# Performance work log

Measured on AMD Instinct MI355X. Metric: run time of the kernel, lower is better.

The kernel has to match this reference:

```python
import jax, jax.numpy as jnp
import numpy as np

B, S, H, L = 128, 2048, 512, 11

def setup_inputs() -> dict:
    key = jax.random.key(0)
    k1, k2, k3, k4 = jax.random.split(key, 4)
    return {
        "find_contri": 1,
        "code_output": jax.random.normal(k1, (B, S, H), dtype=jnp.float32),
        "lengths": jax.random.randint(k2, (B,), 1, S + 1),  # ragged lengths in [1, S]
        "contri": jax.random.uniform(k3, (B, S, 2), dtype=jnp.float32),
        "fc_w": jax.random.normal(k4, (L, H), dtype=jnp.float32) * 0.05,
    }

def reference(find_contri, code_output, lengths, contri, fc_w):
    b, s, h = code_output.shape
    # Faithful to torch .view (reshape, not transpose): [B,S,H] -> [B,H,S]
    x = code_output.reshape(b, h, s)
    # Ragged adaptive max-pool to size 1 with indices: mask positions >= length
    valid = jnp.arange(s)[None, :] < lengths[:, None]            # [B,S]
    xm = jnp.where(valid[:, None, :], x, -jnp.inf)               # [B,H,S]
    code_pool = jnp.max(xm, axis=2)                              # [B,H]
    code_indices = jnp.argmax(xm, axis=2)                        # [B,H], in [0,len)
    attn = code_pool @ fc_w.T                                    # [B,11], no bias
    if find_contri:
        # con[lab,i] = relu(pool[i]*fc_w[lab]) + 1e-4, normalized to sum 100.
        # Original mutates one `contri` tensor across all labs and appends the
        # same reference 11 times; the final state is the sum over labs.
        p10 = code_pool[:10]                                     # only first 10 samples
        con = jax.nn.relu(p10[:, None, :] * fc_w[None, :, :]) + 1e-4   # [10,11,H]
        con = con / jnp.sum(con, axis=2, keepdims=True) * 100.0
        total = jnp.sum(con, axis=1)                             # [10,H]
        # indexed scatter-add into the new third channel
        scat = jax.vmap(lambda idx, c: jnp.zeros((s,), total.dtype).at[idx].add(c))(
            code_indices[:10], total)                            # [10,S]
        ch2 = jnp.zeros((b, s), contri.dtype).at[:10].set(scat)  # [B,S]
        contri_out = jnp.concatenate([contri, ch2[..., None]], axis=2)  # [B,S,3]
        return attn, contri_out
    return attn
```

## Files before the change

kernel.cpp:

```cpp
#include <hip/hip_runtime.h>
#include <math.h>

#define BB 128
#define SS 2048
#define HH 512
#define LL 11

__global__ __launch_bounds__(256) void rowmax_kernel(
    const float* __restrict__ x,
    const int* __restrict__ lengths,
    float* __restrict__ pool,
    int* __restrict__ idx_out) {
  int gid = blockIdx.x * blockDim.x + threadIdx.x;
  int wave = gid >> 6;
  int lane = threadIdx.x & 63;
  if (wave >= BB * HH) return;
  int b = wave >> 9;
  int len = lengths[b];
  const float4* row = (const float4*)(x + (size_t)wave * SS);

  float best = -INFINITY;
  int bidx = 0;
#pragma unroll
  for (int j = 0; j < 8; ++j) {
    int e = j * 64 + lane;
    float4 v = row[e];
    int si = e * 4;
    float a;
    a = (si + 0 < len) ? v.x : -INFINITY;
    if (a > best) { best = a; bidx = si + 0; }
    a = (si + 1 < len) ? v.y : -INFINITY;
    if (a > best) { best = a; bidx = si + 1; }
    a = (si + 2 < len) ? v.z : -INFINITY;
    if (a > best) { best = a; bidx = si + 2; }
    a = (si + 3 < len) ? v.w : -INFINITY;
    if (a > best) { best = a; bidx = si + 3; }
  }
#pragma unroll
  for (int off = 32; off > 0; off >>= 1) {
    float ov = __shfl_down(best, off);
    int oi = __shfl_down(bidx, off);
    if (ov > best || (ov == best && oi < bidx)) { best = ov; bidx = oi; }
  }
  if (lane == 0) {
    pool[wave] = best;
    idx_out[wave] = bidx;
  }
}

__global__ __launch_bounds__(256) void attn_kernel(
    const float* __restrict__ pool,
    const float* __restrict__ fcw,
    float* __restrict__ attn_out) {
  int gid = blockIdx.x * blockDim.x + threadIdx.x;
  int wid = gid >> 6;
  int lane = threadIdx.x & 63;
  if (wid >= BB * LL) return;
  int b = wid / LL;
  int l = wid - b * LL;
  const float* p = pool + b * HH;
  const float* w = fcw + l * HH;
  float sum = 0.f;
#pragma unroll
  for (int k = 0; k < HH / 64; ++k) sum += p[k * 64 + lane] * w[k * 64 + lane];
#pragma unroll
  for (int off = 32; off > 0; off >>= 1) sum += __shfl_down(sum, off);
  if (lane == 0) attn_out[wid] = sum;
}

__global__ __launch_bounds__(256) void denom_kernel(
    const float* __restrict__ pool,
    const float* __restrict__ fcw,
    float* __restrict__ denom) {
  int gid = blockIdx.x * blockDim.x + threadIdx.x;
  int wid = gid >> 6;
  int lane = threadIdx.x & 63;
  if (wid >= 10 * LL) return;
  int b = wid / LL;
  int l = wid - b * LL;
  const float* p = pool + b * HH;
  const float* w = fcw + l * HH;
  float sum = 0.f;
#pragma unroll
  for (int k = 0; k < HH / 64; ++k)
    sum += fmaxf(p[k * 64 + lane] * w[k * 64 + lane], 0.f);
#pragma unroll
  for (int off = 32; off > 0; off >>= 1) sum += __shfl_down(sum, off);
  if (lane == 0) denom[wid] = sum + (float)HH * 1e-4f;
}

__global__ __launch_bounds__(512) void scatter_kernel(
    const float* __restrict__ pool,
    const float* __restrict__ fcw,
    const float* __restrict__ denom,
    const int* __restrict__ idx_in,
    float* __restrict__ ch2) {
  int b = blockIdx.x;
  int hh = threadIdx.x;
  __shared__ float sden[LL];
  if (threadIdx.x < LL) sden[threadIdx.x] = 100.f / denom[b * LL + threadIdx.x];
  __syncthreads();
  float p = pool[b * HH + hh];
  float total = 0.f;
#pragma unroll
  for (int l = 0; l < LL; ++l) {
    float c = fmaxf(p * fcw[l * HH + hh], 0.f) + 1e-4f;
    total += c * sden[l];
  }
  atomicAdd(&ch2[b * SS + idx_in[b * HH + hh]], total);
}

__global__ __launch_bounds__(256) void finalize_kernel(
    const float* __restrict__ contri,
    const float* __restrict__ ch2,
    float* __restrict__ out2) {
  int t = blockIdx.x * blockDim.x + threadIdx.x;
  if (t >= BB * SS) return;
  float c0 = contri[t * 2 + 0];
  float c1 = contri[t * 2 + 1];
  float c2 = (t < 10 * SS) ? ch2[t] : 0.f;
  out2[t * 3 + 0] = c0;
  out2[t * 3 + 1] = c1;
  out2[t * 3 + 2] = c2;
}

extern "C" void kernel_launch(void* const* d_in, const int* in_sizes, int n_in,
                              void* d_out, int out_size, void* d_ws, size_t ws_size,
                              hipStream_t stream) {
  const float* code_output = (const float*)d_in[1];
  const int* lengths = (const int*)d_in[2];
  const float* contri = (const float*)d_in[3];
  const float* fcw = (const float*)d_in[4];

  float* out = (float*)d_out;
  float* out2 = out + BB * LL;

  float* ws = (float*)d_ws;
  float* pool = ws;
  int* idx = (int*)(ws + 65536);
  float* denom = ws + 131072;
  float* ch2 = ws + 131200;

  hipMemsetAsync(ch2, 0, (size_t)10 * SS * sizeof(float), stream);

  rowmax_kernel<<<(BB * HH * 64) / 256, 256, 0, stream>>>(code_output, lengths,
                                                          pool, idx);
  attn_kernel<<<(BB * LL * 64 + 255) / 256, 256, 0, stream>>>(pool, fcw, out);
  denom_kernel<<<(10 * LL * 64 + 255) / 256, 256, 0, stream>>>(pool, fcw, denom);
  scatter_kernel<<<10, 512, 0, stream>>>(pool, fcw, denom, idx, ch2);
  finalize_kernel<<<(BB * SS + 255) / 256, 256, 0, stream>>>(contri, ch2, out2);
}
```

Before: 691.3 us.

## Fuse attn, denom, scatter and finalize into one epilogue kernel; nontemporal row loads

Merges the four small post-reduction kernels and the memset into a single epilogue launch. Block roles are split by block index: the first 10 blocks compute denominators, scatter-add into shared memory and write the contri rows for the first 10 samples; the next 128 blocks compute attn; the remaining blocks copy contri and write zeros. The rowmax streaming loads become nontemporal. This removes several launches plus the global atomic and memset round trips, in exchange for more complex per-block branching and shared-memory atomics.

```diff
diff --git a/kernel.cpp b/kernel.cpp
--- a/kernel.cpp
+++ b/kernel.cpp
@@ -5,6 +5,8 @@
 #define SS 2048
 #define HH 512
 #define LL 11
+
+typedef float vf4 __attribute__((ext_vector_type(4)));
 
 __global__ __launch_bounds__(256) void rowmax_kernel(
     const float* __restrict__ x,
@@ -17,14 +19,14 @@
   if (wave >= BB * HH) return;
   int b = wave >> 9;
   int len = lengths[b];
-  const float4* row = (const float4*)(x + (size_t)wave * SS);
+  const vf4* row = (const vf4*)(x + (size_t)wave * SS);
 
   float best = -INFINITY;
   int bidx = 0;
 #pragma unroll
   for (int j = 0; j < 8; ++j) {
     int e = j * 64 + lane;
-    float4 v = row[e];
+    vf4 v = __builtin_nontemporal_load(&row[e]);
     int si = e * 4;
     float a;
     a = (si + 0 < len) ? v.x : -INFINITY;
@@ -48,80 +50,77 @@
   }
 }
 
-__global__ __launch_bounds__(256) void attn_kernel(
+__global__ __launch_bounds__(256) void epilogue_kernel(
     const float* __restrict__ pool,
+    const int* __restrict__ idx_in,
     const float* __restrict__ fcw,
-    float* __restrict__ attn_out) {
-  int gid = blockIdx.x * blockDim.x + threadIdx.x;
-  int wid = gid >> 6;
-  int lane = threadIdx.x & 63;
-  if (wid >= BB * LL) return;
-  int b = wid / LL;
-  int l = wid - b * LL;
-  const float* p = pool + b * HH;
-  const float* w = fcw + l * HH;
-  float sum = 0.f;
+    const float* __restrict__ contri,
+    float* __restrict__ attn_out,
+    float* __restrict__ out2) {
+  int tid = threadIdx.x;
+  int wv = tid >> 6;
+  int lane = tid & 63;
+
+  if (blockIdx.x < 10) {
+    int b = blockIdx.x;
+    __shared__ float sp[HH];
+    __shared__ float sden[LL];
+    __shared__ float sch[SS];
+
+    for (int h = tid; h < HH; h += 256) sp[h] = pool[b * HH + h];
+    for (int s = tid; s < SS; s += 256) sch[s] = 0.f;
+    __syncthreads();
+
+    for (int l = wv; l < LL; l += 4) {
+      float s = 0.f;
 #pragma unroll
-  for (int k = 0; k < HH / 64; ++k) sum += p[k * 64 + lane] * w[k * 64 + lane];
+      for (int k = 0; k < HH / 64; ++k) {
+        int h = k * 64 + lane;
+        s += fmaxf(sp[h] * fcw[l * HH + h], 0.f);
+      }
 #pragma unroll
-  for (int off = 32; off > 0; off >>= 1) sum += __shfl_down(sum, off);
-  if (lane == 0) attn_out[wid] = sum;
-}
+      for (int off = 32; off > 0; off >>= 1) s += __shfl_down(s, off);
+      if (lane == 0) sden[l] = 100.f / (s + (float)HH * 1e-4f);
+    }
+    __syncthreads();
 
-__global__ __launch_bounds__(256) void denom_kernel(
-    const float* __restrict__ pool,
-    const float* __restrict__ fcw,
-    float* __restrict__ denom) {
-  int gid = blockIdx.x * blockDim.x + threadIdx.x;
-  int wid = gid >> 6;
-  int lane = threadIdx.x & 63;
-  if (wid >= 10 * LL) return;
-  int b = wid / LL;
-  int l = wid - b * LL;
-  const float* p = pool + b * HH;
-  const float* w = fcw + l * HH;
-  float sum = 0.f;
+    for (int hh = tid; hh < HH; hh += 256) {
+      float p = sp[hh];
+      float tot = 0.f;
 #pragma unroll
-  for (int k = 0; k < HH / 64; ++k)
-    sum += fmaxf(p[k * 64 + lane] * w[k * 64 + lane], 0.f);
+      for (int l = 0; l < LL; ++l)
+        tot += (fmaxf(p * fcw[l * HH + hh], 0.f) + 1e-4f) * sden[l];
+      atomicAdd(&sch[idx_in[b * HH + hh]], tot);
+    }
+    __syncthreads();
+
+    for (int s = tid; s < SS; s += 256) {
+      int t = b * SS + s;
+      out2[t * 3 + 0] = contri[t * 2 + 0];
+      out2[t * 3 + 1] = contri[t * 2 + 1];
+      out2[t * 3 + 2] = sch[s];
+    }
+  } else if (blockIdx.x < 10 + BB) {
+    int b = blockIdx.x - 10;
+    const float* p = pool + b * HH;
+    for (int l = wv; l < LL; l += 4) {
+      const float* w = fcw + l * HH;
+      float s = 0.f;
 #pragma unroll
-  for (int off = 32; off > 0; off >>= 1) sum += __shfl_down(sum, off);
-  if (lane == 0) denom[wid] = sum + (float)HH * 1e-4f;
-}
-
-__global__ __launch_bounds__(512) void scatter_kernel(
-    const float* __restrict__ pool,
-    const float* __restrict__ fcw,
-    const float* __restrict__ denom,
-    const int* __restrict__ idx_in,
-    float* __restrict__ ch2) {
-  int b = blockIdx.x;
-  int hh = threadIdx.x;
-  __shared__ float sden[LL];
-  if (threadIdx.x < LL) sden[threadIdx.x] = 100.f / denom[b * LL + threadIdx.x];
-  __syncthreads();
-  float p = pool[b * HH + hh];
-  float total = 0.f;
+      for (int k = 0; k < HH / 64; ++k) s += p[k * 64 + lane] * w[k * 64 + lane];
 #pragma unroll
-  for (int l = 0; l < LL; ++l) {
-    float c = fmaxf(p * fcw[l * HH + hh], 0.f) + 1e-4f;
-    total += c * sden[l];
+      for (int off = 32; off > 0; off >>= 1) s += __shfl_down(s, off);
+      if (lane == 0) attn_out[b * LL + l] = s;
+    }
+  } else {
+    int i = (blockIdx.x - (10 + BB)) * 256 + tid;
+    int t = 10 * SS + i;
+    if (t < BB * SS) {
+      out2[t * 3 + 0] = contri[t * 2 + 0];
+      out2[t * 3 + 1] = contri[t * 2 + 1];
+      out2[t * 3 + 2] = 0.f;
+    }
   }
-  atomicAdd(&ch2[b * SS + idx_in[b * HH + hh]], total);
-}
-
-__global__ __launch_bounds__(256) void finalize_kernel(
-    const float* __restrict__ contri,
-    const float* __restrict__ ch2,
-    float* __restrict__ out2) {
-  int t = blockIdx.x * blockDim.x + threadIdx.x;
-  if (t >= BB * SS) return;
-  float c0 = contri[t * 2 + 0];
-  float c1 = contri[t * 2 + 1];
-  float c2 = (t < 10 * SS) ? ch2[t] : 0.f;
-  out2[t * 3 + 0] = c0;
-  out2[t * 3 + 1] = c1;
-  out2[t * 3 + 2] = c2;
 }
 
 extern "C" void kernel_launch(void* const* d_in, const int* in_sizes, int n_in,
@@ -137,16 +136,12 @@
 
   float* ws = (float*)d_ws;
   float* pool = ws;
-  int* idx = (int*)(ws + 65536);
-  float* denom = ws + 131072;
-  float* ch2 = ws + 131200;
-
-  hipMemsetAsync(ch2, 0, (size_t)10 * SS * sizeof(float), stream);
+  int* idx = (int*)(ws + BB * HH);
 
   rowmax_kernel<<<(BB * HH * 64) / 256, 256, 0, stream>>>(code_output, lengths,
                                                           pool, idx);
-  attn_kernel<<<(BB * LL * 64 + 255) / 256, 256, 0, stream>>>(pool, fcw, out);
-  denom_kernel<<<(10 * LL * 64 + 255) / 256, 256, 0, stream>>>(pool, fcw, denom);
-  scatter_kernel<<<10, 512, 0, stream>>>(pool, fcw, denom, idx, ch2);
-  finalize_kernel<<<(BB * SS + 255) / 256, 256, 0, stream>>>(contri, ch2, out2);
+
+  int copy_blocks = ((BB - 10) * SS + 255) / 256;
+  epilogue_kernel<<<10 + BB + copy_blocks, 256, 0, stream>>>(pool, idx, fcw,
+                                                             contri, out, out2);
 }
```

New measurement: 654.0 us. 5.4% less time.
